# Optimization experiments

Measured on AMD Instinct MI355X. Metric: run time of the kernel, lower is better.

The kernel has to match this reference:

```python
import jax, jax.numpy as jnp
from jax import lax
import numpy as np

N, A, C = 16384, 768, 1000


def setup_inputs() -> dict:
    key = jax.random.key(0)
    k1, k2, k3, k4 = jax.random.split(key, 4)
    return {
        "y": jax.random.normal(k1, (N, C), dtype=jnp.float32),
        "features": jax.random.normal(k2, (N, A), dtype=jnp.float32),
        "fc_weight": jax.random.normal(k3, (C, A), dtype=jnp.float32),
        "labels": jax.random.randint(k4, (N,), 0, C, dtype=jnp.int64),
        "count": jnp.zeros((C,), dtype=jnp.float32),
        "mean": jnp.zeros((C, A), dtype=jnp.float32),
        "cov": jnp.zeros((C, A), dtype=jnp.float32),
        "ratio": jnp.ones((1,), dtype=jnp.float32) * 0.5,
    }


def reference(y, features, fc_weight, labels, count, mean, cov, ratio):
    # ---- EstimatorCV (no-grad per-class mean/var update) ----
    f = lax.stop_gradient(features)                      # (N, A)
    onehot = jax.nn.one_hot(labels, C, dtype=f.dtype)    # (N, C)
    counts = onehot.sum(0)                               # (C,)  per-class sample count
    amount = jnp.maximum(counts, 1.0)[:, None]           # (C, 1) Amount_CxA (0 -> 1)
    sum_f = onehot.T @ f                                 # (C, A) class-wise feature sums
    ave = sum_f / amount                                 # (C, A) ave_CxA
    sum_f2 = onehot.T @ (f * f)                          # (C, A)
    # sum_n onehot[n,c]*(f[n]-ave[c])^2 = sum_f2 - 2*ave*sum_f + counts*ave^2
    var = (sum_f2 - 2.0 * ave * sum_f + counts[:, None] * ave * ave) / amount
    denom = counts + count                               # (C,)
    w = jnp.where(denom > 0, counts / jnp.maximum(denom, 1.0), 0.0)[:, None]  # weight_CV, NaN->0
    new_cov = cov * (1.0 - w) + var * w + w * (1.0 - w) * (mean - ave) ** 2
    new_cov = lax.stop_gradient(new_cov)                 # cov is detached in torch

    # ---- isda_aug: sigma2[n,c] = ratio * sum_a (W[c,a]-W[k_n,a])^2 * cov[k_n,a] ----
    Wm = fc_weight                                       # (C, A)
    cov_n = new_cov[labels]                              # (N, A) gather CV_temp
    w_k = Wm[labels]                                     # (N, A) NxW_kj rows
    term1 = cov_n @ (Wm * Wm).T                          # (N, C) sum_a W[c]^2 * cov_n
    term2 = (w_k * cov_n) @ Wm.T                         # (N, C) sum_a W[c]*w_k*cov_n
    term3 = jnp.sum(w_k * w_k * cov_n, axis=1, keepdims=True)  # (N, 1)
    sigma2 = ratio * (term1 - 2.0 * term2 + term3)       # (N, C)
    return y + 0.5 * sigma2
```

## Files before the change

### kernel.cpp

```cpp
#include <hip/hip_runtime.h>
#include <hip/hip_bf16.h>


constexpr int Nn = 16384;
constexpr int Aa = 768;
constexpr int Cc = 1000;
constexpr int Cp = 1024;
constexpr int Kk = 1536;
constexpr int SLOTS = 64;

using f32x4  = __attribute__((ext_vector_type(4))) float;
using bf16x8 = __attribute__((ext_vector_type(8))) short;

static __device__ inline unsigned short f2bf(float x) {
    __hip_bfloat16 h = __float2bfloat16(x);
    return *reinterpret_cast<unsigned short*>(&h);
}

__global__ __launch_bounds__(256) void scatter_kernel(
    const int* __restrict__ labels, int* __restrict__ cursor, int* __restrict__ order)
{
    int i = blockIdx.x * 256 + threadIdx.x;
    if (i < Nn) {
        int k = labels[i];
        int pos = atomicAdd(&cursor[k], 1);
        if (pos < SLOTS) order[k * SLOTS + pos] = i;
    }
}

__global__ __launch_bounds__(192) void stats_kernel(
    const float4* __restrict__ f4, const int* __restrict__ order,
    const int* __restrict__ cursor, const float* __restrict__ count_in,
    const float4* __restrict__ mean4, const float4* __restrict__ cov4,
    const float4* __restrict__ W4,
    unsigned short* __restrict__ P, unsigned short* __restrict__ Q,
    float* __restrict__ term3)
{
    int c = blockIdx.x;
    int t = threadIdx.x;
    int a = t * 4;
    size_t pq = (size_t)c * Kk;
    if (c >= Cc) {
        ushort4 z = {0, 0, 0, 0};
        *(ushort4*)&P[pq + a] = z; *(ushort4*)&P[pq + Aa + a] = z;
        *(ushort4*)&Q[pq + a] = z; *(ushort4*)&Q[pq + Aa + a] = z;
        return;
    }
    int cntRaw = cursor[c];
    int cnt = min(cntRaw, SLOTS);
    float sf[4] = {0, 0, 0, 0}, sf2[4] = {0, 0, 0, 0};
    const int* ord = order + c * SLOTS;
    int idx = (cnt > 0) ? ord[0] : 0;
    for (int r = 0; r < cnt; ++r) {
        int cur = idx;
        if (r + 1 < cnt) idx = ord[r + 1];
        float4 v = f4[(size_t)cur * 192 + t];
        sf[0] += v.x; sf2[0] += v.x * v.x;
        sf[1] += v.y; sf2[1] += v.y * v.y;
        sf[2] += v.z; sf2[2] += v.z * v.z;
        sf[3] += v.w; sf2[3] += v.w * v.w;
    }
    float cntf = (float)cntRaw;
    float amt = fmaxf(cntf, 1.0f);
    float denom = cntf + count_in[c];
    float w = denom > 0.0f ? cntf / fmaxf(denom, 1.0f) : 0.0f;
    float4 mn = mean4[(size_t)c * 192 + t];
    float4 cv = cov4[(size_t)c * 192 + t];
    float4 wv = W4[(size_t)c * 192 + t];
    float mnA[4] = {mn.x, mn.y, mn.z, mn.w};
    float cvA[4] = {cv.x, cv.y, cv.z, cv.w};
    float wvA[4] = {wv.x, wv.y, wv.z, wv.w};
    ushort4 p0, p1, q0, q1;
    unsigned short* p0a = (unsigned short*)&p0;
    unsigned short* p1a = (unsigned short*)&p1;
    unsigned short* q0a = (unsigned short*)&q0;
    unsigned short* q1a = (unsigned short*)&q1;
    float t3 = 0.0f;
    #pragma unroll
    for (int j = 0; j < 4; ++j) {
        float ave = sf[j] / amt;
        float var = (sf2[j] - 2.0f * ave * sf[j] + cntf * ave * ave) / amt;
        float d = mnA[j] - ave;
        float cov = cvA[j] * (1.0f - w) + var * w + w * (1.0f - w) * d * d;
        float wj = wvA[j];
        p0a[j] = f2bf(cov);
        p1a[j] = f2bf(cov * wj);
        q0a[j] = f2bf(wj * wj);
        q1a[j] = f2bf(-2.0f * wj);
        t3 = fmaf(cov, wj * wj, t3);
    }
    *(ushort4*)&P[pq + a]      = p0;
    *(ushort4*)&P[pq + Aa + a] = p1;
    *(ushort4*)&Q[pq + a]      = q0;
    *(ushort4*)&Q[pq + Aa + a] = q1;
    __shared__ float red[3];
    #pragma unroll
    for (int s = 32; s > 0; s >>= 1) t3 += __shfl_down(t3, s, 64);
    if ((t & 63) == 0) red[t >> 6] = t3;
    __syncthreads();
    if (t == 0) term3[c] = red[0] + red[1] + red[2];
}

__global__ __launch_bounds__(256) void smm_kernel(
    const unsigned short* __restrict__ P, const unsigned short* __restrict__ Q,
    const float* __restrict__ term3, const float* __restrict__ ratio,
    float* __restrict__ S)
{
    constexpr int SST = 72;
    __shared__ unsigned short sP[64 * SST];
    __shared__ unsigned short sQ[64 * SST];
    int t = threadIdx.x;
    int w = t >> 6, l = t & 63;
    int quad = l >> 4, l16 = l & 15;
    int wr = w >> 1, wc = w & 1;
    int kbase = blockIdx.y * 64;
    int cbase = blockIdx.x * 64;

    int row0 = t >> 3, row1 = row0 + 32, g = t & 7;
    const unsigned short* pSrc0 = P + (size_t)(kbase + row0) * Kk + g * 8;
    const unsigned short* pSrc1 = P + (size_t)(kbase + row1) * Kk + g * 8;
    const unsigned short* qSrc0 = Q + (size_t)(cbase + row0) * Kk + g * 8;
    const unsigned short* qSrc1 = Q + (size_t)(cbase + row1) * Kk + g * 8;
    unsigned short* pDst0 = &sP[row0 * SST + g * 8];
    unsigned short* pDst1 = &sP[row1 * SST + g * 8];
    unsigned short* qDst0 = &sQ[row0 * SST + g * 8];
    unsigned short* qDst1 = &sQ[row1 * SST + g * 8];

    uint4 pv0 = *(const uint4*)pSrc0;
    uint4 pv1 = *(const uint4*)pSrc1;
    uint4 qv0 = *(const uint4*)qSrc0;
    uint4 qv1 = *(const uint4*)qSrc1;

    f32x4 acc[2][2] = {};
    constexpr int NCH = Kk / 64;
    for (int it = 0; it < NCH; ++it) {
        __syncthreads();
        *(uint4*)pDst0 = pv0;
        *(uint4*)pDst1 = pv1;
        *(uint4*)qDst0 = qv0;
        *(uint4*)qDst1 = qv1;
        __syncthreads();
        if (it + 1 < NCH) {
            int k0 = (it + 1) * 64;
            pv0 = *(const uint4*)(pSrc0 + k0);
            pv1 = *(const uint4*)(pSrc1 + k0);
            qv0 = *(const uint4*)(qSrc0 + k0);
            qv1 = *(const uint4*)(qSrc1 + k0);
        }
        #pragma unroll
        for (int kstep = 0; kstep < 2; ++kstep) {
            bf16x8 aF[2], bF[2];
            #pragma unroll
            for (int mt = 0; mt < 2; ++mt)
                aF[mt] = *(const bf16x8*)&sP[(wr * 32 + mt * 16 + l16) * SST
                                             + kstep * 32 + quad * 8];
            #pragma unroll
            for (int nt = 0; nt < 2; ++nt)
                bF[nt] = *(const bf16x8*)&sQ[(wc * 32 + nt * 16 + l16) * SST
                                             + kstep * 32 + quad * 8];
            #pragma unroll
            for (int mt = 0; mt < 2; ++mt)
                #pragma unroll
                for (int nt = 0; nt < 2; ++nt)
                    acc[mt][nt] = __builtin_amdgcn_mfma_f32_16x16x32_bf16(
                        aF[mt], bF[nt], acc[mt][nt], 0, 0, 0);
        }
    }
    float r = ratio[0];
    #pragma unroll
    for (int mt = 0; mt < 2; ++mt) {
        int krow0 = kbase + wr * 32 + mt * 16 + quad * 4;
        #pragma unroll
        for (int nt = 0; nt < 2; ++nt) {
            int ccol = cbase + wc * 32 + nt * 16 + l16;
            if (ccol < Cc) {
                #pragma unroll
                for (int reg = 0; reg < 4; ++reg) {
                    int k = krow0 + reg;
                    if (k < Cc)
                        S[(size_t)k * Cc + ccol] = r * (acc[mt][nt][reg] + term3[k]);
                }
            }
        }
    }
}

__global__ __launch_bounds__(256) void out_kernel(
    const f32x4* __restrict__ y4, const int* __restrict__ labels,
    const float* __restrict__ S, f32x4* __restrict__ out4)
{
    const unsigned total4 = (unsigned)Nn * 250u;
    unsigned base = blockIdx.x * 512u + threadIdx.x;
    #pragma unroll
    for (int half = 0; half < 2; ++half) {
        unsigned i = base + (unsigned)half * 256u;
        if (i < total4) {
            unsigned n = i / 250u;
            unsigned c4 = i - n * 250u;
            int k = labels[n];
            f32x4 yv = __builtin_nontemporal_load(&y4[i]);
            const f32x4* srow = (const f32x4*)(S + (size_t)k * Cc);
            f32x4 sv = srow[c4];
            f32x4 o = yv + 0.5f * sv;
            __builtin_nontemporal_store(o, &out4[i]);
        }
    }
}

extern "C" void kernel_launch(void* const* d_in, const int* in_sizes, int n_in,
                              void* d_out, int out_size, void* d_ws, size_t ws_size,
                              hipStream_t stream) {
    const float* y        = (const float*)d_in[0];
    const float* features = (const float*)d_in[1];
    const float* fc_w     = (const float*)d_in[2];
    const int*   labels   = (const int*)d_in[3];
    const float* count_in = (const float*)d_in[4];
    const float* mean_in  = (const float*)d_in[5];
    const float* cov_in   = (const float*)d_in[6];
    const float* ratio    = (const float*)d_in[7];

    char* base = (char*)d_ws;
    int*   cursor = (int*)base;
    float* term3  = (float*)(base + 4096);
    int*   order  = (int*)(base + 8192);
    unsigned short* P = (unsigned short*)(base + 8192 + Cp * SLOTS * 4);
    unsigned short* Q = P + (size_t)Cp * Kk;
    float* S = (float*)(Q + (size_t)Cp * Kk);

    hipMemsetAsync(cursor, 0, 4096, stream);

    scatter_kernel<<<(Nn + 255) / 256, 256, 0, stream>>>(labels, cursor, order);

    stats_kernel<<<Cp, 192, 0, stream>>>(
        (const float4*)features, order, cursor, count_in,
        (const float4*)mean_in, (const float4*)cov_in, (const float4*)fc_w,
        P, Q, term3);

    dim3 gS(Cp / 64, Cp / 64);
    smm_kernel<<<gS, 256, 0, stream>>>(P, Q, term3, ratio, S);

    const unsigned total4 = (unsigned)Nn * 250u;
    out_kernel<<<(total4 + 511) / 512, 256, 0, stream>>>(
        (const f32x4*)y, labels, S, (f32x4*)d_out);
}
```

Measured before the change: 203.5 us.

## Fuse label scatter into stats kernel and double-buffer LDS in class GEMM

Removes the memset and the separate scatter kernel. Each stats block now scans the full label array and builds its class's sample list in shared memory with shared atomics. This cuts two launches and the global atomics, at the cost of every block re-reading all labels. The class-by-class GEMM also switches to double-buffered shared tiles, which drops one barrier per K chunk and overlaps global prefetch with MFMA work.

Result: faster. 194.6 us (-4.3%).

```diff
diff --git a/kernel.cpp b/kernel.cpp
--- a/kernel.cpp
+++ b/kernel.cpp
@@ -17,20 +17,9 @@
     return *reinterpret_cast<unsigned short*>(&h);
 }
 
-__global__ __launch_bounds__(256) void scatter_kernel(
-    const int* __restrict__ labels, int* __restrict__ cursor, int* __restrict__ order)
-{
-    int i = blockIdx.x * 256 + threadIdx.x;
-    if (i < Nn) {
-        int k = labels[i];
-        int pos = atomicAdd(&cursor[k], 1);
-        if (pos < SLOTS) order[k * SLOTS + pos] = i;
-    }
-}
-
 __global__ __launch_bounds__(192) void stats_kernel(
-    const float4* __restrict__ f4, const int* __restrict__ order,
-    const int* __restrict__ cursor, const float* __restrict__ count_in,
+    const float4* __restrict__ f4, const int* __restrict__ labels,
+    const float* __restrict__ count_in,
     const float4* __restrict__ mean4, const float4* __restrict__ cov4,
     const float4* __restrict__ W4,
     unsigned short* __restrict__ P, unsigned short* __restrict__ Q,
@@ -46,14 +35,28 @@
         *(ushort4*)&Q[pq + a] = z; *(ushort4*)&Q[pq + Aa + a] = z;
         return;
     }
-    int cntRaw = cursor[c];
+    __shared__ int list[SLOTS];
+    __shared__ int s_cnt;
+    __shared__ float red[3];
+    if (t == 0) s_cnt = 0;
+    __syncthreads();
+    const int4* lab4 = (const int4*)labels;
+    for (int j = t; j < Nn / 4; j += 192) {
+        int4 v = lab4[j];
+        if (v.x == c) { int p = atomicAdd(&s_cnt, 1); if (p < SLOTS) list[p] = 4 * j;     }
+        if (v.y == c) { int p = atomicAdd(&s_cnt, 1); if (p < SLOTS) list[p] = 4 * j + 1; }
+        if (v.z == c) { int p = atomicAdd(&s_cnt, 1); if (p < SLOTS) list[p] = 4 * j + 2; }
+        if (v.w == c) { int p = atomicAdd(&s_cnt, 1); if (p < SLOTS) list[p] = 4 * j + 3; }
+    }
+    __syncthreads();
+    int cntRaw = s_cnt;
     int cnt = min(cntRaw, SLOTS);
+
     float sf[4] = {0, 0, 0, 0}, sf2[4] = {0, 0, 0, 0};
-    const int* ord = order + c * SLOTS;
-    int idx = (cnt > 0) ? ord[0] : 0;
+    int idx = (cnt > 0) ? list[0] : 0;
     for (int r = 0; r < cnt; ++r) {
         int cur = idx;
-        if (r + 1 < cnt) idx = ord[r + 1];
+        if (r + 1 < cnt) idx = list[r + 1];
         float4 v = f4[(size_t)cur * 192 + t];
         sf[0] += v.x; sf2[0] += v.x * v.x;
         sf[1] += v.y; sf2[1] += v.y * v.y;
@@ -93,7 +96,6 @@
     *(ushort4*)&P[pq + Aa + a] = p1;
     *(ushort4*)&Q[pq + a]      = q0;
     *(ushort4*)&Q[pq + Aa + a] = q1;
-    __shared__ float red[3];
     #pragma unroll
     for (int s = 32; s > 0; s >>= 1) t3 += __shfl_down(t3, s, 64);
     if ((t & 63) == 0) red[t >> 6] = t3;
@@ -107,8 +109,9 @@
     float* __restrict__ S)
 {
     constexpr int SST = 72;
-    __shared__ unsigned short sP[64 * SST];
-    __shared__ unsigned short sQ[64 * SST];
+    constexpr int BUF = 64 * SST;
+    __shared__ unsigned short sP[2 * BUF];
+    __shared__ unsigned short sQ[2 * BUF];
     int t = threadIdx.x;
     int w = t >> 6, l = t & 63;
     int quad = l >> 4, l16 = l & 15;
@@ -121,42 +124,39 @@
     const unsigned short* pSrc1 = P + (size_t)(kbase + row1) * Kk + g * 8;
     const unsigned short* qSrc0 = Q + (size_t)(cbase + row0) * Kk + g * 8;
     const unsigned short* qSrc1 = Q + (size_t)(cbase + row1) * Kk + g * 8;
-    unsigned short* pDst0 = &sP[row0 * SST + g * 8];
-    unsigned short* pDst1 = &sP[row1 * SST + g * 8];
-    unsigned short* qDst0 = &sQ[row0 * SST + g * 8];
-    unsigned short* qDst1 = &sQ[row1 * SST + g * 8];
+    int dOff0 = row0 * SST + g * 8;
+    int dOff1 = row1 * SST + g * 8;
 
     uint4 pv0 = *(const uint4*)pSrc0;
     uint4 pv1 = *(const uint4*)pSrc1;
     uint4 qv0 = *(const uint4*)qSrc0;
     uint4 qv1 = *(const uint4*)qSrc1;
+    *(uint4*)&sP[dOff0] = pv0;
+    *(uint4*)&sP[dOff1] = pv1;
+    *(uint4*)&sQ[dOff0] = qv0;
+    *(uint4*)&sQ[dOff1] = qv1;
+    pv0 = *(const uint4*)(pSrc0 + 64);
+    pv1 = *(const uint4*)(pSrc1 + 64);
+    qv0 = *(const uint4*)(qSrc0 + 64);
+    qv1 = *(const uint4*)(qSrc1 + 64);
+    __syncthreads();
 
     f32x4 acc[2][2] = {};
     constexpr int NCH = Kk / 64;
     for (int it = 0; it < NCH; ++it) {
-        __syncthreads();
-        *(uint4*)pDst0 = pv0;
-        *(uint4*)pDst1 = pv1;
-        *(uint4*)qDst0 = qv0;
-        *(uint4*)qDst1 = qv1;
-        __syncthreads();
-        if (it + 1 < NCH) {
-            int k0 = (it + 1) * 64;
-            pv0 = *(const uint4*)(pSrc0 + k0);
-            pv1 = *(const uint4*)(pSrc1 + k0);
-            qv0 = *(const uint4*)(qSrc0 + k0);
-            qv1 = *(const uint4*)(qSrc1 + k0);
-        }
+        int cur = it & 1;
+        const unsigned short* bP = &sP[cur * BUF];
+        const unsigned short* bQ = &sQ[cur * BUF];
         #pragma unroll
         for (int kstep = 0; kstep < 2; ++kstep) {
             bf16x8 aF[2], bF[2];
             #pragma unroll
             for (int mt = 0; mt < 2; ++mt)
-                aF[mt] = *(const bf16x8*)&sP[(wr * 32 + mt * 16 + l16) * SST
+                aF[mt] = *(const bf16x8*)&bP[(wr * 32 + mt * 16 + l16) * SST
                                              + kstep * 32 + quad * 8];
             #pragma unroll
             for (int nt = 0; nt < 2; ++nt)
-                bF[nt] = *(const bf16x8*)&sQ[(wc * 32 + nt * 16 + l16) * SST
+                bF[nt] = *(const bf16x8*)&bQ[(wc * 32 + nt * 16 + l16) * SST
                                              + kstep * 32 + quad * 8];
             #pragma unroll
             for (int mt = 0; mt < 2; ++mt)
@@ -165,6 +165,21 @@
                     acc[mt][nt] = __builtin_amdgcn_mfma_f32_16x16x32_bf16(
                         aF[mt], bF[nt], acc[mt][nt], 0, 0, 0);
         }
+        if (it + 1 < NCH) {
+            int nb = (cur ^ 1) * BUF;
+            *(uint4*)&sP[nb + dOff0] = pv0;
+            *(uint4*)&sP[nb + dOff1] = pv1;
+            *(uint4*)&sQ[nb + dOff0] = qv0;
+            *(uint4*)&sQ[nb + dOff1] = qv1;
+            if (it + 2 < NCH) {
+                int k0 = (it + 2) * 64;
+                pv0 = *(const uint4*)(pSrc0 + k0);
+                pv1 = *(const uint4*)(pSrc1 + k0);
+                qv0 = *(const uint4*)(qSrc0 + k0);
+                qv1 = *(const uint4*)(qSrc1 + k0);
+            }
+        }
+        __syncthreads();
     }
     float r = ratio[0];
     #pragma unroll
@@ -220,19 +235,13 @@
     const float* ratio    = (const float*)d_in[7];
 
     char* base = (char*)d_ws;
-    int*   cursor = (int*)base;
-    float* term3  = (float*)(base + 4096);
-    int*   order  = (int*)(base + 8192);
-    unsigned short* P = (unsigned short*)(base + 8192 + Cp * SLOTS * 4);
+    float* term3 = (float*)base;
+    unsigned short* P = (unsigned short*)(base + 4096);
     unsigned short* Q = P + (size_t)Cp * Kk;
     float* S = (float*)(Q + (size_t)Cp * Kk);
 
-    hipMemsetAsync(cursor, 0, 4096, stream);
-
-    scatter_kernel<<<(Nn + 255) / 256, 256, 0, stream>>>(labels, cursor, order);
-
     stats_kernel<<<Cp, 192, 0, stream>>>(
-        (const float4*)features, order, cursor, count_in,
+        (const float4*)features, labels, count_in,
         (const float4*)mean_in, (const float4*)cov_in, (const float4*)fc_w,
         P, Q, term3);
 
```
